# Kernel tuning notes

Measured on AMD Instinct MI355X. Metric: run time of the kernel, lower is better.

Reference implementation:

```python
import jax, jax.numpy as jnp
import numpy as np

N, E, D, H, C = 100000, 1600000, 128, 256, 40


def setup_inputs() -> dict:
    key = jax.random.key(0)
    ks = jax.random.split(key, 10)
    x = jax.random.normal(ks[0], (N, D), dtype=jnp.float32)
    src = jax.random.randint(ks[1], (E,), 0, N, dtype=jnp.int32)
    dst = jax.random.randint(ks[2], (E,), 0, N, dtype=jnp.int32)
    # GIN layer 1 MLP (bias-free), kaiming-uniform-like scale 1/sqrt(fan_in)
    w1a = jax.random.normal(ks[3], (D, H), dtype=jnp.float32) / np.sqrt(D)
    w1b = jax.random.normal(ks[4], (H, H), dtype=jnp.float32) / np.sqrt(H)
    # GIN layer 2 MLP
    w2a = jax.random.normal(ks[5], (H, H), dtype=jnp.float32) / np.sqrt(H)
    w2b = jax.random.normal(ks[6], (H, H), dtype=jnp.float32) / np.sqrt(H)
    # eps initialized to 0 per reset_parameters
    eps1 = jnp.zeros((), dtype=jnp.float32)
    eps2 = jnp.zeros((), dtype=jnp.float32)
    # final classifier fc (with bias)
    fc_w = jax.random.normal(ks[7], (H, C), dtype=jnp.float32) / np.sqrt(H)
    fc_b = jax.random.normal(ks[8], (C,), dtype=jnp.float32) * 0.01
    return {"x": x, "src": src, "dst": dst,
            "eps1": eps1, "w1a": w1a, "w1b": w1b,
            "eps2": eps2, "w2a": w2a, "w2b": w2b,
            "fc_w": fc_w, "fc_b": fc_b}


def reference(x, src, dst, eps1, w1a, w1b, eps2, w2a, w2b, fc_w, fc_b):
    n = x.shape[0]

    def gin_layer(h, eps, wa, wb):
        # GINConv sum-aggregation: scatter-add neighbor feats over edges
        agg = jax.ops.segment_sum(h[src], dst, num_segments=n)  # [N, d]
        rst = (1.0 + eps) * h + agg
        # 2-layer bias-free MLP with ReLU between
        return jax.nn.relu(rst @ wa) @ wb

    h = jax.nn.relu(gin_layer(x, eps1, w1a, w1b))   # layer + outer activation
    h = jax.nn.relu(gin_layer(h, eps2, w2a, w2b))   # dropout p=0 -> identity
    return h @ fc_w + fc_b                           # [N, C]
```

## Files before the change

### kernel.cpp

```cpp
#include <hip/hip_runtime.h>

#define N_NODES 100000
#define N_EDGES 1600000
#define DIM_IN  128
#define DIM_H   256
#define DIM_C   40

#define NB   391
#define NBLK 391
#define CHUNK 4096
#define ECAP 6144

typedef unsigned short bf16_t;
typedef __attribute__((ext_vector_type(8))) short short8;
typedef __attribute__((ext_vector_type(4))) float f32x4;

__device__ __forceinline__ bf16_t f2b(float f) {
    unsigned int u = __float_as_uint(f);
    unsigned int r = (u + 0x7fffu + ((u >> 16) & 1u)) >> 16;
    return (bf16_t)r;
}
__device__ __forceinline__ float b2f(unsigned int h16) {
    return __uint_as_float(h16 << 16);
}

__device__ __forceinline__ void gl_lds16(const void* gsrc, void* ldst) {
    __builtin_amdgcn_global_load_lds(
        (const __attribute__((address_space(1))) void*)gsrc,
        (__attribute__((address_space(3))) void*)ldst,
        16, 0, 0);
}


__global__ void k_bhist(const int* __restrict__ dst, int* __restrict__ cnt2, int e) {
    __shared__ int h[NB];
    int t = threadIdx.x, blk = blockIdx.x;
    for (int i = t; i < NB; i += 256) h[i] = 0;
    __syncthreads();
    int base = blk * CHUNK;
    int end = min(base + CHUNK, e);
    for (int i = base + t; i < end; i += 256)
        atomicAdd(&h[dst[i] >> 8], 1);
    __syncthreads();
    for (int i = t; i < NB; i += 256) cnt2[blk * NB + i] = h[i];
}

__global__ void k_bscanA(const int* __restrict__ cnt2, int* __restrict__ basep,
                         int* __restrict__ btot) {
    __shared__ int s[512];
    int t = threadIdx.x, b = blockIdx.x;
    int v = (t < NBLK) ? cnt2[t * NB + b] : 0;
    s[t] = v;
    __syncthreads();
    #pragma unroll
    for (int d = 1; d < 512; d <<= 1) {
        int tv = (t >= d) ? s[t - d] : 0;
        __syncthreads();
        s[t] += tv;
        __syncthreads();
    }
    if (t < NBLK) basep[t * NB + b] = s[t] - v;
    if (t == 511) btot[b] = s[511];
}

__global__ void k_bscan2(const int* __restrict__ btot, int* __restrict__ boff) {
    __shared__ int s[512];
    int t = threadIdx.x;
    int v = (t < NB) ? btot[t] : 0;
    s[t] = v;
    __syncthreads();
    #pragma unroll
    for (int d = 1; d < 512; d <<= 1) {
        int tv = (t >= d) ? s[t - d] : 0;
        __syncthreads();
        s[t] += tv;
        __syncthreads();
    }
    if (t < NB) boff[t] = s[t] - v;
    if (t == NB - 1) boff[NB] = s[t];
}

__global__ void k_bscatter(const int* __restrict__ src, const int* __restrict__ dst,
                           const int* __restrict__ basep, const int* __restrict__ boff,
                           int* __restrict__ ebuf, int e) {
    __shared__ int cur[NB];
    int t = threadIdx.x, blk = blockIdx.x;
    for (int i = t; i < NB; i += 256) cur[i] = basep[blk * NB + i] + boff[i];
    __syncthreads();
    int base = blk * CHUNK;
    int end = min(base + CHUNK, e);
    for (int i = base + t; i < end; i += 256) {
        int sv = src[i], dv = dst[i];
        int pos = atomicAdd(&cur[dv >> 8], 1);
        ebuf[pos] = sv | ((dv & 255) << 24);
    }
}

__global__ __launch_bounds__(256) void k_build(const int* __restrict__ ebuf,
                                               const int* __restrict__ boff,
                                               int* __restrict__ off,
                                               int* __restrict__ csr) {
    __shared__ int ec[ECAP];
    __shared__ int h[256];
    __shared__ int cur[256];
    int t = threadIdx.x, b = blockIdx.x;
    int node0 = b << 8;
    int e0 = boff[b], e1 = boff[b + 1];
    int ne = e1 - e0;
    bool fits = (ne <= ECAP);
    h[t] = 0;
    __syncthreads();
    if (fits) {
        for (int i = t; i < ne; i += 256) {
            int p = ebuf[e0 + i];
            ec[i] = p;
            atomicAdd(&h[(unsigned)p >> 24], 1);
        }
    } else {
        for (int i = t; i < ne; i += 256)
            atomicAdd(&h[(unsigned)ebuf[e0 + i] >> 24], 1);
    }
    __syncthreads();
    int mydeg = h[t];
    #pragma unroll
    for (int d = 1; d < 256; d <<= 1) {
        int tv = (t >= d) ? h[t - d] : 0;
        __syncthreads();
        h[t] += tv;
        __syncthreads();
    }
    int node = node0 + t;
    if (node < N_NODES) off[node + 1] = e0 + h[t];
    if (b == 0 && t == 0) off[0] = 0;
    cur[t] = e0 + h[t] - mydeg;
    __syncthreads();
    if (fits) {
        for (int i = t; i < ne; i += 256) {
            int p = ec[i];
            int pos = atomicAdd(&cur[(unsigned)p >> 24], 1);
            csr[pos] = p & 0xFFFFFF;
        }
    } else {
        for (int i = t; i < ne; i += 256) {
            int p = ebuf[e0 + i];
            int pos = atomicAdd(&cur[(unsigned)p >> 24], 1);
            csr[pos] = p & 0xFFFFFF;
        }
    }
}


__global__ void k_cvt_i8(const float* __restrict__ x, signed char* __restrict__ x8,
                         float* __restrict__ xs, int n) {
    int gid = blockIdx.x * blockDim.x + threadIdx.x;
    int u = gid >> 6, lane = gid & 63;
    if (u >= n) return;
    float2 v = *(const float2*)(x + (size_t)u * 128 + lane * 2);
    float m = fmaxf(fabsf(v.x), fabsf(v.y));
    #pragma unroll
    for (int d = 1; d < 64; d <<= 1)
        m = fmaxf(m, __shfl_xor(m, d, 64));
    float inv = (m > 0.f) ? 127.f / m : 0.f;
    int q0 = (int)rintf(v.x * inv);
    int q1 = (int)rintf(v.y * inv);
    unsigned short pk = (unsigned short)((q0 & 0xff) | ((q1 & 0xff) << 8));
    *(unsigned short*)(x8 + ((unsigned)u << 7) + lane * 2) = pk;
    if (lane == 0) xs[u] = (m > 0.f) ? m * (1.f / 127.f) : 0.f;
}

__global__ void k_wcvt(const float* __restrict__ w1a, const float* __restrict__ w1b,
                       const float* __restrict__ w2a, const float* __restrict__ w2b,
                       const float* __restrict__ fcw,
                       bf16_t* __restrict__ o1a, bf16_t* __restrict__ o1b,
                       bf16_t* __restrict__ o2a, bf16_t* __restrict__ o2b,
                       bf16_t* __restrict__ ofc) {
    int r = blockIdx.y;
    int idx = blockIdx.x * 256 + threadIdx.x;
    const float* in; bf16_t* out; int K, N, Npad;
    switch (r) {
        case 0: in = w1a; out = o1a; K = 128; N = 256; Npad = 256; break;
        case 1: in = w1b; out = o1b; K = 256; N = 256; Npad = 256; break;
        case 2: in = w2a; out = o2a; K = 256; N = 256; Npad = 256; break;
        case 3: in = w2b; out = o2b; K = 256; N = 256; Npad = 256; break;
        default: in = fcw; out = ofc; K = 256; N = 40;  Npad = 128; break;
    }
    if (idx >= Npad * K) return;
    int n = idx / K, k = idx - n * K;
    float v = (n < N) ? in[(size_t)k * N + n] : 0.f;
    out[idx] = f2b(v);
}


__global__ void k_agg_i8(const signed char* __restrict__ h8, const float* __restrict__ hs,
                         const int* __restrict__ off, const int* __restrict__ csr,
                         const float* __restrict__ eps_p,
                         bf16_t* __restrict__ rst, int n) {
    int gid = blockIdx.x * blockDim.x + threadIdx.x;
    int u = __builtin_amdgcn_readfirstlane(gid >> 6);
    int lane = threadIdx.x & 63;
    if (u >= n) return;

    float acc0 = 0.f, acc1 = 0.f;
    int r0 = off[u], r1 = off[u + 1];
    int r = r0;
    unsigned loff = lane * 2u;
    for (; r + 8 <= r1; r += 8) {
        int s[8];
        #pragma unroll
        for (int t = 0; t < 8; t++) s[t] = __builtin_amdgcn_readfirstlane(csr[r + t]);
        float sc[8];
        #pragma unroll
        for (int t = 0; t < 8; t++) sc[t] = hs[s[t]];
        unsigned v[8];
        #pragma unroll
        for (int t = 0; t < 8; t++)
            v[t] = *(const unsigned short*)(h8 + (((unsigned)s[t] << 7) + loff));
        #pragma unroll
        for (int t = 0; t < 8; t++) {
            acc0 += (float)(int)(signed char)(v[t] & 0xffu) * sc[t];
            acc1 += (float)(int)(signed char)(v[t] >> 8) * sc[t];
        }
    }
    for (; r < r1; r++) {
        int s = __builtin_amdgcn_readfirstlane(csr[r]);
        float sc = hs[s];
        unsigned v = *(const unsigned short*)(h8 + (((unsigned)s << 7) + loff));
        acc0 += (float)(int)(signed char)(v & 0xffu) * sc;
        acc1 += (float)(int)(signed char)(v >> 8) * sc;
    }

    float scu = hs[u] * (1.0f + eps_p[0]);
    unsigned vu = *(const unsigned short*)(h8 + (((unsigned)u << 7) + loff));
    float o0 = (float)(int)(signed char)(vu & 0xffu) * scu + acc0;
    float o1 = (float)(int)(signed char)(vu >> 8) * scu + acc1;
    *(unsigned int*)(rst + ((unsigned)u << 7) + lane * 2) =
        (unsigned int)f2b(o0) | ((unsigned int)f2b(o1) << 16);
}


__global__ void k_agg_u8(const unsigned char* __restrict__ h8,
                         const float* __restrict__ hs,
                         const int* __restrict__ off, const int* __restrict__ csr,
                         const float* __restrict__ eps_p,
                         bf16_t* __restrict__ rst, int n) {
    int gid = blockIdx.x * blockDim.x + threadIdx.x;
    int u = __builtin_amdgcn_readfirstlane(gid >> 6);
    int lane = threadIdx.x & 63;
    if (u >= n) return;

    float acc[4] = {0.f, 0.f, 0.f, 0.f};
    int r0 = off[u], r1 = off[u + 1];
    int r = r0;
    unsigned loff = lane * 4u;
    for (; r + 8 <= r1; r += 8) {
        int s[8];
        #pragma unroll
        for (int t = 0; t < 8; t++) s[t] = __builtin_amdgcn_readfirstlane(csr[r + t]);
        float sc[8];
        #pragma unroll
        for (int t = 0; t < 8; t++) sc[t] = hs[s[t]];
        unsigned int v[8];
        #pragma unroll
        for (int t = 0; t < 8; t++)
            v[t] = *(const unsigned int*)(h8 + (((unsigned)s[t] << 8) + loff));
        #pragma unroll
        for (int t = 0; t < 8; t++) {
            acc[0] += (float)(v[t] & 0xffu) * sc[t];
            acc[1] += (float)((v[t] >> 8) & 0xffu) * sc[t];
            acc[2] += (float)((v[t] >> 16) & 0xffu) * sc[t];
            acc[3] += (float)(v[t] >> 24) * sc[t];
        }
    }
    for (; r < r1; r++) {
        int s = __builtin_amdgcn_readfirstlane(csr[r]);
        float sc = hs[s];
        unsigned int v = *(const unsigned int*)(h8 + (((unsigned)s << 8) + loff));
        acc[0] += (float)(v & 0xffu) * sc;
        acc[1] += (float)((v >> 8) & 0xffu) * sc;
        acc[2] += (float)((v >> 16) & 0xffu) * sc;
        acc[3] += (float)(v >> 24) * sc;
    }

    float ep = 1.0f + eps_p[0];
    unsigned int vu = *(const unsigned int*)(h8 + (((unsigned)u << 8) + loff));
    float scu = hs[u] * ep;
    float o0 = (float)(vu & 0xffu) * scu + acc[0];
    float o1 = (float)((vu >> 8) & 0xffu) * scu + acc[1];
    float o2 = (float)((vu >> 16) & 0xffu) * scu + acc[2];
    float o3 = (float)(vu >> 24) * scu + acc[3];
    uint2 ov;
    ov.x = (unsigned int)f2b(o0) | ((unsigned int)f2b(o1) << 16);
    ov.y = (unsigned int)f2b(o2) | ((unsigned int)f2b(o3) << 16);
    *(uint2*)(rst + (size_t)u * 256 + lane * 4) = ov;
}


#define TS_STRIDE 264

template <int K1, bool OUT8>
__global__ __launch_bounds__(256, 2) void k_mlp(
    const bf16_t* __restrict__ A, const bf16_t* __restrict__ W1t,
    const bf16_t* __restrict__ W2t, bf16_t* __restrict__ H,
    unsigned char* __restrict__ H8, float* __restrict__ Hs, int M)
{
    __shared__ __align__(16) bf16_t As[64 * 32];
    __shared__ __align__(16) bf16_t Bs[256 * 32];
    __shared__ __align__(16) bf16_t Ts[64 * TS_STRIDE];
    __shared__ int rmax[64];

    int tid = threadIdx.x;
    int wave = tid >> 6, lane = tid & 63;
    int l15 = lane & 15, quad = lane >> 4;
    int bm = blockIdx.x * 64;
    int wn = wave * 64;

    f32x4 acc[4][4];
    #pragma unroll
    for (int i = 0; i < 4; i++)
        #pragma unroll
        for (int j = 0; j < 4; j++) acc[i][j] = 0.f;

    for (int k0 = 0; k0 < K1; k0 += 32) {
        {
            int row = tid >> 2, k8 = (tid & 3) * 8;
            int gr = bm + row; if (gr >= M) gr = M - 1;
            gl_lds16(A + (size_t)gr * K1 + k0 + k8, &As[(wave * 64) * 8]);
        }
        #pragma unroll
        for (int l = 0; l < 4; l++) {
            int s = l * 256 + tid;
            int row = s >> 2, k8 = (s & 3) * 8;
            gl_lds16(W1t + (size_t)row * K1 + k0 + k8, &Bs[(size_t)(l * 256 + wave * 64) * 8]);
        }
        __syncthreads();

        short8 af[4], bfv[4];
        #pragma unroll
        for (int i = 0; i < 4; i++)
            af[i] = *(const short8*)&As[(i * 16 + l15) * 32 + quad * 8];
        #pragma unroll
        for (int j = 0; j < 4; j++)
            bfv[j] = *(const short8*)&Bs[(wn + j * 16 + l15) * 32 + quad * 8];

        #pragma unroll
        for (int i = 0; i < 4; i++)
            #pragma unroll
            for (int j = 0; j < 4; j++)
                acc[i][j] = __builtin_amdgcn_mfma_f32_16x16x32_bf16(af[i], bfv[j], acc[i][j], 0, 0, 0);
        __syncthreads();
    }

    #pragma unroll
    for (int i = 0; i < 4; i++)
        #pragma unroll
        for (int j = 0; j < 4; j++) {
            int row = i * 16 + quad * 4;
            int col = wn + j * 16 + l15;
            #pragma unroll
            for (int r = 0; r < 4; r++)
                Ts[(row + r) * TS_STRIDE + col] = f2b(fmaxf(acc[i][j][r], 0.f));
        }

    #pragma unroll
    for (int i = 0; i < 4; i++)
        #pragma unroll
        for (int j = 0; j < 4; j++) acc[i][j] = 0.f;
    __syncthreads();

    for (int k0 = 0; k0 < 256; k0 += 32) {
        #pragma unroll
        for (int l = 0; l < 4; l++) {
            int s = l * 256 + tid;
            int row = s >> 2, k8 = (s & 3) * 8;
            gl_lds16(W2t + (size_t)row * 256 + k0 + k8, &Bs[(size_t)(l * 256 + wave * 64) * 8]);
        }
        __syncthreads();

        short8 af[4], bfv[4];
        #pragma unroll
        for (int i = 0; i < 4; i++)
            af[i] = *(const short8*)&Ts[(i * 16 + l15) * TS_STRIDE + k0 + quad * 8];
        #pragma unroll
        for (int j = 0; j < 4; j++)
            bfv[j] = *(const short8*)&Bs[(wn + j * 16 + l15) * 32 + quad * 8];

        #pragma unroll
        for (int i = 0; i < 4; i++)
            #pragma unroll
            for (int j = 0; j < 4; j++)
                acc[i][j] = __builtin_amdgcn_mfma_f32_16x16x32_bf16(af[i], bfv[j], acc[i][j], 0, 0, 0);
        __syncthreads();
    }

    if constexpr (OUT8) {
        if (tid < 64) rmax[tid] = 0;
        __syncthreads();
        #pragma unroll
        for (int i = 0; i < 4; i++)
            #pragma unroll
            for (int r = 0; r < 4; r++) {
                float m = 0.f;
                #pragma unroll
                for (int j = 0; j < 4; j++) m = fmaxf(m, acc[i][j][r]);
                atomicMax(&rmax[i * 16 + quad * 4 + r], __float_as_int(m));
            }
        __syncthreads();
        #pragma unroll
        for (int i = 0; i < 4; i++) {
            #pragma unroll
            for (int r = 0; r < 4; r++) {
                int row = i * 16 + quad * 4 + r;
                int rowg = bm + row;
                if (rowg >= M) continue;
                float rm = __int_as_float(rmax[row]);
                float inv = (rm > 0.f) ? 255.f / rm : 0.f;
                #pragma unroll
                for (int j = 0; j < 4; j++) {
                    int col = wn + j * 16 + l15;
                    float v = fmaxf(acc[i][j][r], 0.f);
                    unsigned q = (unsigned)(v * inv + 0.5f);
                    if (q > 255u) q = 255u;
                    H8[(size_t)rowg * 256 + col] = (unsigned char)q;
                }
                if (wave == 0 && l15 == 0)
                    Hs[rowg] = rm * (1.f / 255.f);
            }
        }
    } else {
        #pragma unroll
        for (int j = 0; j < 4; j++) {
            int col = wn + j * 16 + l15;
            #pragma unroll
            for (int i = 0; i < 4; i++) {
                #pragma unroll
                for (int r = 0; r < 4; r++) {
                    int rowg = bm + i * 16 + quad * 4 + r;
                    if (rowg < M)
                        H[(size_t)rowg * 256 + col] = f2b(fmaxf(acc[i][j][r], 0.f));
                }
            }
        }
    }
}


__global__ __launch_bounds__(256) void gemm_fc(
    const bf16_t* __restrict__ A, const bf16_t* __restrict__ Bt,
    const float* __restrict__ bias, float* __restrict__ C,
    int M, int K, int Nst)
{
    __shared__ __align__(16) bf16_t As[128 * 32];
    __shared__ __align__(16) bf16_t Bs[128 * 32];

    int tid = threadIdx.x;
    int wave = tid >> 6, lane = tid & 63;
    int l15 = lane & 15, quad = lane >> 4;
    int bm = blockIdx.y * 128, bn = blockIdx.x * 128;
    int wm = (wave >> 1) * 64, wn = (wave & 1) * 64;

    f32x4 acc[4][4];
    #pragma unroll
    for (int i = 0; i < 4; i++)
        #pragma unroll
        for (int j = 0; j < 4; j++) acc[i][j] = 0.f;

    for (int k0 = 0; k0 < K; k0 += 32) {
        #pragma unroll
        for (int iss = 0; iss < 2; iss++) {
            int s = iss * 256 + wave * 64 + lane;
            int row = s >> 2;
            int k8 = (s & 3) * 8;
            int ldsoff = (iss * 256 + wave * 64) * 8;

            int grA = bm + row; if (grA >= M) grA = M - 1;
            gl_lds16(A + (size_t)grA * K + k0 + k8, &As[ldsoff]);

            int grB = bn + row;
            gl_lds16(Bt + (size_t)grB * K + k0 + k8, &Bs[ldsoff]);
        }
        __syncthreads();

        short8 af[4], bfv[4];
        #pragma unroll
        for (int i = 0; i < 4; i++)
            af[i] = *(const short8*)&As[(wm + i * 16 + l15) * 32 + quad * 8];
        #pragma unroll
        for (int j = 0; j < 4; j++)
            bfv[j] = *(const short8*)&Bs[(wn + j * 16 + l15) * 32 + quad * 8];

        #pragma unroll
        for (int i = 0; i < 4; i++)
            #pragma unroll
            for (int j = 0; j < 4; j++)
                acc[i][j] = __builtin_amdgcn_mfma_f32_16x16x32_bf16(af[i], bfv[j], acc[i][j], 0, 0, 0);
        __syncthreads();
    }

    #pragma unroll
    for (int j = 0; j < 4; j++) {
        int col = bn + wn + j * 16 + l15;
        if (col >= Nst) continue;
        float bv = bias[col];
        #pragma unroll
        for (int i = 0; i < 4; i++) {
            #pragma unroll
            for (int r = 0; r < 4; r++) {
                int rowg = bm + wm + i * 16 + quad * 4 + r;
                if (rowg < M)
                    C[(size_t)rowg * Nst + col] = acc[i][j][r] + bv;
            }
        }
    }
}


static inline size_t rnd256(size_t x) { return (x + 255) & ~(size_t)255; }

extern "C" void kernel_launch(void* const* d_in, const int* in_sizes, int n_in,
                              void* d_out, int out_size, void* d_ws, size_t ws_size,
                              hipStream_t stream) {
    const float* x    = (const float*)d_in[0];
    const int*   src  = (const int*)d_in[1];
    const int*   dst  = (const int*)d_in[2];
    const float* eps1 = (const float*)d_in[3];
    const float* w1a  = (const float*)d_in[4];
    const float* w1b  = (const float*)d_in[5];
    const float* eps2 = (const float*)d_in[6];
    const float* w2a  = (const float*)d_in[7];
    const float* w2b  = (const float*)d_in[8];
    const float* fc_w = (const float*)d_in[9];
    const float* fc_b = (const float*)d_in[10];
    float* out = (float*)d_out;

    char* w = (char*)d_ws;
    int* off  = (int*)w; w += rnd256(sizeof(int) * (size_t)(N_NODES + 1));
    int* csr  = (int*)w; w += rnd256(sizeof(int) * (size_t)N_EDGES);
    int* cnt2  = (int*)w; w += rnd256(sizeof(int) * (size_t)NBLK * NB);
    int* basep = (int*)w; w += rnd256(sizeof(int) * (size_t)NBLK * NB);
    int* btot  = (int*)w; w += rnd256(sizeof(int) * 512);
    int* boff  = (int*)w; w += rnd256(sizeof(int) * (NB + 1));
    bf16_t* w1a_t = (bf16_t*)w; w += rnd256(2 * (size_t)DIM_H * DIM_IN);
    bf16_t* w1b_t = (bf16_t*)w; w += rnd256(2 * (size_t)DIM_H * DIM_H);
    bf16_t* w2a_t = (bf16_t*)w; w += rnd256(2 * (size_t)DIM_H * DIM_H);
    bf16_t* w2b_t = (bf16_t*)w; w += rnd256(2 * (size_t)DIM_H * DIM_H);
    bf16_t* fc_t  = (bf16_t*)w; w += rnd256(2 * (size_t)128 * DIM_H);
    signed char* x8 = (signed char*)w; w += rnd256((size_t)N_NODES * DIM_IN);
    float* xs = (float*)w; w += rnd256(sizeof(float) * (size_t)N_NODES);
    unsigned char* h8 = (unsigned char*)w; w += rnd256((size_t)N_NODES * DIM_H);
    float* hs = (float*)w; w += rnd256(sizeof(float) * (size_t)N_NODES);
    bf16_t* R12 = (bf16_t*)w; w += rnd256(2 * (size_t)N_NODES * DIM_H);
    bf16_t* R3  = (bf16_t*)w; w += rnd256(2 * (size_t)N_NODES * DIM_H);

    bf16_t* rst1 = R12;
    int* ebuf = (int*)R3;

    k_bhist<<<NBLK, 256, 0, stream>>>(dst, cnt2, N_EDGES);
    k_bscanA<<<NB, 512, 0, stream>>>(cnt2, basep, btot);
    k_bscan2<<<1, 512, 0, stream>>>(btot, boff);
    k_bscatter<<<NBLK, 256, 0, stream>>>(src, dst, basep, boff, ebuf, N_EDGES);
    k_build<<<NB, 256, 0, stream>>>(ebuf, boff, off, csr);

    k_cvt_i8<<<(N_NODES * 64 + 255) / 256, 256, 0, stream>>>(x, x8, xs, N_NODES);
    {
        dim3 g(256, 5);
        k_wcvt<<<g, 256, 0, stream>>>(w1a, w1b, w2a, w2b, fc_w,
                                      w1a_t, w1b_t, w2a_t, w2b_t, fc_t);
    }

    const int agg_blocks = (N_NODES * 64 + 255) / 256;
    const int mlp_blocks = (N_NODES + 63) / 64;

    k_agg_i8<<<agg_blocks, 256, 0, stream>>>(x8, xs, off, csr, eps1, rst1, N_NODES);
    k_mlp<DIM_IN, true><<<mlp_blocks, 256, 0, stream>>>(rst1, w1a_t, w1b_t,
                                                        nullptr, h8, hs, N_NODES);

    k_agg_u8<<<agg_blocks, 256, 0, stream>>>(h8, hs, off, csr, eps2, (bf16_t*)R3, N_NODES);
    k_mlp<DIM_H, false><<<mlp_blocks, 256, 0, stream>>>((bf16_t*)R3, w2a_t, w2b_t,
                                                        R12, nullptr, nullptr, N_NODES);

    dim3 g1(1, (N_NODES + 127) / 128);
    gemm_fc<<<g1, 256, 0, stream>>>(R12, fc_t, fc_b, out, N_NODES, DIM_H, DIM_C);
}
```

Before: 443.0 us.

## Split aggregation over feature slices and parallelize edges across lanes

Both aggregation kernels now split each node's feature row into 8 column slices handled by separate blocks. Within a wave, lanes are grouped so several edges are gathered in parallel (16 edges for int8 layer, 8 for uint8 layer), then reduced with xor shuffles. This replaces the serial per-edge loop with wave-uniform indices, aiming for more memory-level parallelism per wave. The cost is 8x more blocks, repeated CSR and scale loads per slice, shuffle reductions, and narrower per-row gathers, with only some lanes writing the result.

```diff
diff --git a/kernel.cpp b/kernel.cpp
--- a/kernel.cpp
+++ b/kernel.cpp
@@ -195,46 +195,47 @@
                          const int* __restrict__ off, const int* __restrict__ csr,
                          const float* __restrict__ eps_p,
                          bf16_t* __restrict__ rst, int n) {
-    int gid = blockIdx.x * blockDim.x + threadIdx.x;
-    int u = __builtin_amdgcn_readfirstlane(gid >> 6);
+    int b = blockIdx.x;
+    int slice = b & 7;
+    int u = __builtin_amdgcn_readfirstlane(((b >> 3) << 2) + (int)(threadIdx.x >> 6));
+    if (u >= n) return;
     int lane = threadIdx.x & 63;
-    if (u >= n) return;
-
-    float acc0 = 0.f, acc1 = 0.f;
+    int t = lane >> 2, d = lane & 3;
+    unsigned coff = (unsigned)slice * 16u + (unsigned)d * 4u;
+
+    float a0 = 0.f, a1 = 0.f, a2 = 0.f, a3 = 0.f;
     int r0 = off[u], r1 = off[u + 1];
-    int r = r0;
-    unsigned loff = lane * 2u;
-    for (; r + 8 <= r1; r += 8) {
-        int s[8];
-        #pragma unroll
-        for (int t = 0; t < 8; t++) s[t] = __builtin_amdgcn_readfirstlane(csr[r + t]);
-        float sc[8];
-        #pragma unroll
-        for (int t = 0; t < 8; t++) sc[t] = hs[s[t]];
-        unsigned v[8];
-        #pragma unroll
-        for (int t = 0; t < 8; t++)
-            v[t] = *(const unsigned short*)(h8 + (((unsigned)s[t] << 7) + loff));
-        #pragma unroll
-        for (int t = 0; t < 8; t++) {
-            acc0 += (float)(int)(signed char)(v[t] & 0xffu) * sc[t];
-            acc1 += (float)(int)(signed char)(v[t] >> 8) * sc[t];
-        }
-    }
-    for (; r < r1; r++) {
-        int s = __builtin_amdgcn_readfirstlane(csr[r]);
+    int lim = r1 - 1;
+    for (int r = r0; r < r1; r += 16) {
+        int e = min(r + t, lim);
+        int s = csr[e];
         float sc = hs[s];
-        unsigned v = *(const unsigned short*)(h8 + (((unsigned)s << 7) + loff));
-        acc0 += (float)(int)(signed char)(v & 0xffu) * sc;
-        acc1 += (float)(int)(signed char)(v >> 8) * sc;
-    }
-
-    float scu = hs[u] * (1.0f + eps_p[0]);
-    unsigned vu = *(const unsigned short*)(h8 + (((unsigned)u << 7) + loff));
-    float o0 = (float)(int)(signed char)(vu & 0xffu) * scu + acc0;
-    float o1 = (float)(int)(signed char)(vu >> 8) * scu + acc1;
-    *(unsigned int*)(rst + ((unsigned)u << 7) + lane * 2) =
-        (unsigned int)f2b(o0) | ((unsigned int)f2b(o1) << 16);
+        if (r + t >= r1) sc = 0.f;
+        unsigned v = *(const unsigned*)(h8 + (((unsigned)s << 7) + coff));
+        a0 += (float)(int)(signed char)(v & 0xffu) * sc;
+        a1 += (float)(int)(signed char)((v >> 8) & 0xffu) * sc;
+        a2 += (float)(int)(signed char)((v >> 16) & 0xffu) * sc;
+        a3 += (float)(int)(signed char)(v >> 24) * sc;
+    }
+    #pragma unroll
+    for (int m = 4; m < 64; m <<= 1) {
+        a0 += __shfl_xor(a0, m, 64);
+        a1 += __shfl_xor(a1, m, 64);
+        a2 += __shfl_xor(a2, m, 64);
+        a3 += __shfl_xor(a3, m, 64);
+    }
+    if (t == 0) {
+        float scu = hs[u] * (1.0f + eps_p[0]);
+        unsigned vu = *(const unsigned*)(h8 + (((unsigned)u << 7) + coff));
+        float o0 = (float)(int)(signed char)(vu & 0xffu) * scu + a0;
+        float o1 = (float)(int)(signed char)((vu >> 8) & 0xffu) * scu + a1;
+        float o2 = (float)(int)(signed char)((vu >> 16) & 0xffu) * scu + a2;
+        float o3 = (float)(int)(signed char)(vu >> 24) * scu + a3;
+        uint2 ov;
+        ov.x = (unsigned)f2b(o0) | ((unsigned)f2b(o1) << 16);
+        ov.y = (unsigned)f2b(o2) | ((unsigned)f2b(o3) << 16);
+        *(uint2*)(rst + ((unsigned)u << 7) + slice * 16 + d * 4) = ov;
+    }
 }
 
 
@@ -243,55 +244,47 @@
                          const int* __restrict__ off, const int* __restrict__ csr,
                          const float* __restrict__ eps_p,
                          bf16_t* __restrict__ rst, int n) {
-    int gid = blockIdx.x * blockDim.x + threadIdx.x;
-    int u = __builtin_amdgcn_readfirstlane(gid >> 6);
+    int b = blockIdx.x;
+    int slice = b & 7;
+    int u = __builtin_amdgcn_readfirstlane(((b >> 3) << 2) + (int)(threadIdx.x >> 6));
+    if (u >= n) return;
     int lane = threadIdx.x & 63;
-    if (u >= n) return;
-
-    float acc[4] = {0.f, 0.f, 0.f, 0.f};
+    int t = lane >> 3, d = lane & 7;
+    unsigned coff = (unsigned)slice * 32u + (unsigned)d * 4u;
+
+    float a0 = 0.f, a1 = 0.f, a2 = 0.f, a3 = 0.f;
     int r0 = off[u], r1 = off[u + 1];
-    int r = r0;
-    unsigned loff = lane * 4u;
-    for (; r + 8 <= r1; r += 8) {
-        int s[8];
-        #pragma unroll
-        for (int t = 0; t < 8; t++) s[t] = __builtin_amdgcn_readfirstlane(csr[r + t]);
-        float sc[8];
-        #pragma unroll
-        for (int t = 0; t < 8; t++) sc[t] = hs[s[t]];
-        unsigned int v[8];
-        #pragma unroll
-        for (int t = 0; t < 8; t++)
-            v[t] = *(const unsigned int*)(h8 + (((unsigned)s[t] << 8) + loff));
-        #pragma unroll
-        for (int t = 0; t < 8; t++) {
-            acc[0] += (float)(v[t] & 0xffu) * sc[t];
-            acc[1] += (float)((v[t] >> 8) & 0xffu) * sc[t];
-            acc[2] += (float)((v[t] >> 16) & 0xffu) * sc[t];
-            acc[3] += (float)(v[t] >> 24) * sc[t];
-        }
-    }
-    for (; r < r1; r++) {
-        int s = __builtin_amdgcn_readfirstlane(csr[r]);
+    int lim = r1 - 1;
+    for (int r = r0; r < r1; r += 8) {
+        int e = min(r + t, lim);
+        int s = csr[e];
         float sc = hs[s];
-        unsigned int v = *(const unsigned int*)(h8 + (((unsigned)s << 8) + loff));
-        acc[0] += (float)(v & 0xffu) * sc;
-        acc[1] += (float)((v >> 8) & 0xffu) * sc;
-        acc[2] += (float)((v >> 16) & 0xffu) * sc;
-        acc[3] += (float)(v >> 24) * sc;
-    }
-
-    float ep = 1.0f + eps_p[0];
-    unsigned int vu = *(const unsigned int*)(h8 + (((unsigned)u << 8) + loff));
-    float scu = hs[u] * ep;
-    float o0 = (float)(vu & 0xffu) * scu + acc[0];
-    float o1 = (float)((vu >> 8) & 0xffu) * scu + acc[1];
-    float o2 = (float)((vu >> 16) & 0xffu) * scu + acc[2];
-    float o3 = (float)(vu >> 24) * scu + acc[3];
-    uint2 ov;
-    ov.x = (unsigned int)f2b(o0) | ((unsigned int)f2b(o1) << 16);
-    ov.y = (unsigned int)f2b(o2) | ((unsigned int)f2b(o3) << 16);
-    *(uint2*)(rst + (size_t)u * 256 + lane * 4) = ov;
+        if (r + t >= r1) sc = 0.f;
+        unsigned v = *(const unsigned*)(h8 + (((unsigned)s << 8) + coff));
+        a0 += (float)(v & 0xffu) * sc;
+        a1 += (float)((v >> 8) & 0xffu) * sc;
+        a2 += (float)((v >> 16) & 0xffu) * sc;
+        a3 += (float)(v >> 24) * sc;
+    }
+    #pragma unroll
+    for (int m = 8; m < 64; m <<= 1) {
+        a0 += __shfl_xor(a0, m, 64);
+        a1 += __shfl_xor(a1, m, 64);
+        a2 += __shfl_xor(a2, m, 64);
+        a3 += __shfl_xor(a3, m, 64);
+    }
+    if (t == 0) {
+        float scu = hs[u] * (1.0f + eps_p[0]);
+        unsigned vu = *(const unsigned*)(h8 + (((unsigned)u << 8) + coff));
+        float o0 = (float)(vu & 0xffu) * scu + a0;
+        float o1 = (float)((vu >> 8) & 0xffu) * scu + a1;
+        float o2 = (float)((vu >> 16) & 0xffu) * scu + a2;
+        float o3 = (float)(vu >> 24) * scu + a3;
+        uint2 ov;
+        ov.x = (unsigned)f2b(o0) | ((unsigned)f2b(o1) << 16);
+        ov.y = (unsigned)f2b(o2) | ((unsigned)f2b(o3) << 16);
+        *(uint2*)(rst + (size_t)u * 256 + slice * 32 + d * 4) = ov;
+    }
 }
 
 
@@ -567,7 +560,7 @@
                                       w1a_t, w1b_t, w2a_t, w2b_t, fc_t);
     }
 
-    const int agg_blocks = (N_NODES * 64 + 255) / 256;
+    const int agg_blocks = 8 * ((N_NODES + 3) / 4);
     const int mlp_blocks = (N_NODES + 63) / 64;
 
     k_agg_i8<<<agg_blocks, 256, 0, stream>>>(x8, xs, off, csr, eps1, rst1, N_NODES);
```

Measured after the change: 931.5 us. +110.3%, slower.
